# Kernel tuning notes

Measured on AMD Instinct MI355X. Metric: run time of the kernel, lower is better.

Reference implementation:

```python
import jax, jax.numpy as jnp
import numpy as np

ATT = 256
NUM_GENES = 2128
HIDDEN = 512
B, T = 128, 1024


def setup_inputs() -> dict:
    key = jax.random.key(0)
    ks = jax.random.split(key, 8)
    return {
        "genes": jax.random.normal(ks[0], (B, NUM_GENES), dtype=jnp.float32),
        "smiles": jax.random.normal(ks[1], (B, T, HIDDEN), dtype=jnp.float32),
        "w_num_gene_features": jax.random.normal(ks[2], (1,), dtype=jnp.float32) * 0.1,
        "w_genes": jax.random.normal(ks[3], (NUM_GENES, ATT), dtype=jnp.float32) * 0.1,
        "b_genes": jax.random.normal(ks[4], (ATT,), dtype=jnp.float32) * 0.1,
        "dense_kernel": jax.random.normal(ks[5], (HIDDEN, ATT), dtype=jnp.float32) * 0.05,
        "dense_bias": jnp.zeros((ATT,), dtype=jnp.float32),
        "v": jax.random.normal(ks[6], (ATT,), dtype=jnp.float32) * 0.1,
    }


def reference(genes, smiles, w_num_gene_features, w_genes, b_genes,
              dense_kernel, dense_bias, v):
    # genes: [B, G]; collapse trivial feature axis via scalar weight -> [B, G]
    genes_collapsed = genes * w_num_gene_features[0]
    # gene context: [B, A]
    gene_proj = genes_collapsed @ w_genes + b_genes
    # smiles projection: [B, T, A]
    smiles_proj = jnp.einsum('bth,ha->bta', smiles, dense_kernel) + dense_bias
    # additive attention energies
    x = jnp.tanh(gene_proj[:, None, :] + smiles_proj)          # [B, T, A]
    xv = jnp.einsum('bta,a->bt', x, v)                          # [B, T]
    alphas = jax.nn.softmax(xv, axis=-1)                        # [B, T]
    output = jnp.einsum('bth,bt->bh', smiles, alphas)           # [B, H]
    return output, alphas
```

## Files before the change

kernel.cpp:

```cpp
#include <hip/hip_runtime.h>
#include <stdint.h>

#define B_ 128
#define T_ 1024
#define H_ 512
#define A_ 256
#define G_ 2128

typedef short s16x8 __attribute__((ext_vector_type(8)));
typedef float f32x4 __attribute__((ext_vector_type(4)));
typedef unsigned int u32;

__device__ inline unsigned short f2bf(float f) {
  unsigned u = __float_as_uint(f);
  u += 0x7fff + ((u >> 16) & 1);
  return (unsigned short)(u >> 16);
}
__device__ inline unsigned pack2bf(float a, float b) {
  return ((unsigned)f2bf(b) << 16) | f2bf(a);
}
__device__ inline float bf_lo(unsigned u) { return __uint_as_float(u << 16); }
__device__ inline float bf_hi(unsigned u) { return __uint_as_float(u & 0xffff0000u); }
__device__ inline float fast_tanh(float x) {
  x = fminf(15.f, fmaxf(-15.f, x));
  float e = __expf(2.f * x);
  return (e - 1.f) * __builtin_amdgcn_rcpf(e + 1.f);
}
__device__ inline void gl_lds16(const void* g, void* l) {
  __builtin_amdgcn_global_load_lds(
      (const __attribute__((address_space(1))) u32*)g,
      (__attribute__((address_space(3))) u32*)l, 16, 0, 0);
}

__global__ void prep_kt(const float* __restrict__ K,
                        unsigned short* __restrict__ khi) {
  int idx = blockIdx.x * 256 + threadIdx.x;
  int h = idx >> 8;
  int a = idx & 255;
  int kb = h >> 5, k = h & 31;
  int grp = k >> 3, sub = k & 7;
  khi[kb * 8192 + a * 32 + ((grp ^ (a & 3)) * 8) + sub] = f2bf(K[idx]);
}

__global__ __launch_bounds__(256) void gene_proj_k(
    const float* __restrict__ genes, const float* __restrict__ w0p,
    const float* __restrict__ Wg, const float* __restrict__ bg,
    const float* __restrict__ db, float* __restrict__ gp) {
  __shared__ float sg[532];
  int b = blockIdx.x;
  int gc = blockIdx.y;
  int a = threadIdx.x;
  int g0 = gc * 532;
  for (int i = threadIdx.x; i < 532; i += 256) sg[i] = genes[(size_t)b * G_ + g0 + i];
  __syncthreads();
  float s = 0.f;
  #pragma unroll 8
  for (int g = 0; g < 532; ++g)
    s = fmaf(sg[g], Wg[(size_t)(g0 + g) * A_ + a], s);
  float val = w0p[0] * s;
  if (gc == 0) val += bg[a] + db[a];
  atomicAdd(&gp[b * A_ + a], val);
}

__global__ __launch_bounds__(256, 4) void pass1(
    const float* __restrict__ smiles, const unsigned short* __restrict__ khi,
    unsigned short* __restrict__ smb, const float* __restrict__ gp,
    const float* __restrict__ v, float* __restrict__ xv) {
  __shared__ unsigned short sA[64 * 32];
  __shared__ unsigned short sB[256 * 32];
  __shared__ float sXV[64 * 4];

  const int tid = threadIdx.x;
  const int b = blockIdx.y;
  const int tb = blockIdx.x;
  const int lane = tid & 63;
  const int w = tid >> 6;
  const int n = lane & 15;
  const int q = lane >> 4;

  const int ar = tid >> 2;
  const int ac = tid & 3;
  const int swg = (ac ^ (ar & 3)) * 8;
  const float* asrc = smiles + ((size_t)(b * 1024 + tb * 64 + ar)) * 512 + ac * 8;
  unsigned short* adst =
      smb + ((((size_t)(b * 16 + tb)) * 16 * 64 + ar) * 32) + swg;

  f32x4 acc[4][4];
  #pragma unroll
  for (int i = 0; i < 4; ++i)
    #pragma unroll
    for (int j = 0; j < 4; ++j)
      acc[i][j] = (f32x4){0.f, 0.f, 0.f, 0.f};

  float4 f0 = *reinterpret_cast<const float4*>(asrc);
  float4 f1 = *reinterpret_cast<const float4*>(asrc + 4);

  for (int kb = 0; kb < 16; ++kb) {
    __syncthreads();
    uint4 p;
    p.x = pack2bf(f0.x, f0.y); p.y = pack2bf(f0.z, f0.w);
    p.z = pack2bf(f1.x, f1.y); p.w = pack2bf(f1.z, f1.w);
    *reinterpret_cast<uint4*>(&sA[ar * 32 + swg]) = p;
    *reinterpret_cast<uint4*>(adst + kb * 2048) = p;
    #pragma unroll
    for (int r = 0; r < 4; ++r)
      gl_lds16(khi + kb * 8192 + w * 2048 + r * 512 + lane * 8,
               &sB[w * 2048 + r * 512]);
    __syncthreads();
    if (kb < 15) {
      f0 = *reinterpret_cast<const float4*>(asrc + (kb + 1) * 32);
      f1 = *reinterpret_cast<const float4*>(asrc + (kb + 1) * 32 + 4);
    }

    s16x8 af[4], bh[4];
    const int sw = (q ^ (n & 3)) * 8;
    #pragma unroll
    for (int i = 0; i < 4; ++i)
      af[i] = *reinterpret_cast<const s16x8*>(&sA[(i * 16 + n) * 32 + sw]);
    #pragma unroll
    for (int j = 0; j < 4; ++j)
      bh[j] = *reinterpret_cast<const s16x8*>(&sB[(w * 64 + j * 16 + n) * 32 + sw]);
    #pragma unroll
    for (int i = 0; i < 4; ++i)
      #pragma unroll
      for (int j = 0; j < 4; ++j)
        acc[i][j] = __builtin_amdgcn_mfma_f32_16x16x32_bf16(af[i], bh[j], acc[i][j], 0, 0, 0);
  }

  float vv[4], gg[4];
  #pragma unroll
  for (int j = 0; j < 4; ++j) {
    int a = w * 64 + j * 16 + n;
    vv[j] = v[a];
    gg[j] = gp[b * A_ + a];
  }
  #pragma unroll
  for (int i = 0; i < 4; ++i) {
    #pragma unroll
    for (int r = 0; r < 4; ++r) {
      float s = 0.f;
      #pragma unroll
      for (int j = 0; j < 4; ++j)
        s += vv[j] * fast_tanh(acc[i][j][r] + gg[j]);
      s += __shfl_xor(s, 1); s += __shfl_xor(s, 2);
      s += __shfl_xor(s, 4); s += __shfl_xor(s, 8);
      if (n == 0) sXV[(i * 16 + q * 4 + r) * 4 + w] = s;
    }
  }
  __syncthreads();
  if (tid < 64) {
    float* p = &sXV[tid * 4];
    xv[(size_t)b * T_ + tb * 64 + tid] = p[0] + p[1] + p[2] + p[3];
  }
}

__global__ __launch_bounds__(256) void softmax_k(const float* __restrict__ xv,
                                                 float* __restrict__ alphas) {
  __shared__ float red[8];
  int b = blockIdx.x, tid = threadIdx.x;
  float4 x = *reinterpret_cast<const float4*>(xv + b * T_ + tid * 4);
  float m = fmaxf(fmaxf(x.x, x.y), fmaxf(x.z, x.w));
  #pragma unroll
  for (int o = 1; o < 64; o <<= 1) m = fmaxf(m, __shfl_xor(m, o));
  if ((tid & 63) == 0) red[tid >> 6] = m;
  __syncthreads();
  m = fmaxf(fmaxf(red[0], red[1]), fmaxf(red[2], red[3]));
  float e0 = __expf(x.x - m), e1 = __expf(x.y - m);
  float e2 = __expf(x.z - m), e3 = __expf(x.w - m);
  float s = e0 + e1 + e2 + e3;
  #pragma unroll
  for (int o = 1; o < 64; o <<= 1) s += __shfl_xor(s, o);
  if ((tid & 63) == 0) red[4 + (tid >> 6)] = s;
  __syncthreads();
  s = red[4] + red[5] + red[6] + red[7];
  float inv = 1.f / s;
  float4 o4;
  o4.x = e0 * inv; o4.y = e1 * inv; o4.z = e2 * inv; o4.w = e3 * inv;
  *reinterpret_cast<float4*>(alphas + b * T_ + tid * 4) = o4;
}

__global__ __launch_bounds__(256) void pass3(const unsigned short* __restrict__ smb,
                                             const float* __restrict__ alphas,
                                             float* __restrict__ out) {
  __shared__ float red[3][64][8];
  int b = blockIdx.y, ts = blockIdx.x;
  int tid = threadIdx.x;
  int hg = tid & 63, tq = tid >> 6;
  int kb = hg >> 2, g = hg & 3;
  float acc[8] = {0.f, 0.f, 0.f, 0.f, 0.f, 0.f, 0.f, 0.f};
  for (int tb = ts * 4; tb < ts * 4 + 4; ++tb) {
    const unsigned short* tile = smb + (((size_t)b * 16 + tb) * 16 + kb) * 2048;
    const float* al = alphas + b * T_ + tb * 64;
    #pragma unroll 4
    for (int tt = 0; tt < 16; ++tt) {
      int tp = tq * 16 + tt;
      float a = al[tp];
      uint4 d = *reinterpret_cast<const uint4*>(tile + tp * 32 + ((g ^ (tp & 3)) * 8));
      acc[0] = fmaf(a, bf_lo(d.x), acc[0]); acc[1] = fmaf(a, bf_hi(d.x), acc[1]);
      acc[2] = fmaf(a, bf_lo(d.y), acc[2]); acc[3] = fmaf(a, bf_hi(d.y), acc[3]);
      acc[4] = fmaf(a, bf_lo(d.z), acc[4]); acc[5] = fmaf(a, bf_hi(d.z), acc[5]);
      acc[6] = fmaf(a, bf_lo(d.w), acc[6]); acc[7] = fmaf(a, bf_hi(d.w), acc[7]);
    }
  }
  if (tq) {
    #pragma unroll
    for (int e = 0; e < 8; ++e) red[tq - 1][hg][e] = acc[e];
  }
  __syncthreads();
  if (tq == 0) {
    float* op = out + (size_t)b * H_ + kb * 32 + g * 8;
    #pragma unroll
    for (int e = 0; e < 8; ++e)
      atomicAdd(op + e, acc[e] + red[0][hg][e] + red[1][hg][e] + red[2][hg][e]);
  }
}

extern "C" void kernel_launch(void* const* d_in, const int* in_sizes, int n_in,
                              void* d_out, int out_size, void* d_ws, size_t ws_size,
                              hipStream_t stream) {
  const float* genes  = (const float*)d_in[0];
  const float* smiles = (const float*)d_in[1];
  const float* w0     = (const float*)d_in[2];
  const float* wg     = (const float*)d_in[3];
  const float* bg     = (const float*)d_in[4];
  const float* dk     = (const float*)d_in[5];
  const float* db     = (const float*)d_in[6];
  const float* v      = (const float*)d_in[7];
  float* out = (float*)d_out;
  char* ws = (char*)d_ws;
  float* gp = (float*)ws;
  unsigned short* khi = (unsigned short*)(ws + 131072);
  float* xv = (float*)(ws + 131072 + 262144);
  unsigned short* smb = (unsigned short*)(ws + (1 << 20));
  float* alphas = out + B_ * H_;

  hipMemsetAsync(gp, 0, B_ * A_ * sizeof(float), stream);
  hipMemsetAsync(out, 0, B_ * H_ * sizeof(float), stream);
  prep_kt<<<512, 256, 0, stream>>>(dk, khi);
  gene_proj_k<<<dim3(B_, 4), 256, 0, stream>>>(genes, w0, wg, bg, db, gp);
  pass1<<<dim3(16, B_), 256, 0, stream>>>(smiles, khi, smb, gp, v, xv);
  softmax_k<<<B_, 256, 0, stream>>>(xv, alphas);
  pass3<<<dim3(4, B_), 256, 0, stream>>>(smb, alphas, out);
}
```

Before: 507.3 us.

## Double pass1 row tile to 128 and replace gene_proj atomics with partial buffers

```diff
diff --git a/kernel.cpp b/kernel.cpp
--- a/kernel.cpp
+++ b/kernel.cpp
@@ -45,7 +45,7 @@
 __global__ __launch_bounds__(256) void gene_proj_k(
     const float* __restrict__ genes, const float* __restrict__ w0p,
     const float* __restrict__ Wg, const float* __restrict__ bg,
-    const float* __restrict__ db, float* __restrict__ gp) {
+    const float* __restrict__ db, float* __restrict__ gp4) {
   __shared__ float sg[532];
   int b = blockIdx.x;
   int gc = blockIdx.y;
@@ -59,16 +59,16 @@
     s = fmaf(sg[g], Wg[(size_t)(g0 + g) * A_ + a], s);
   float val = w0p[0] * s;
   if (gc == 0) val += bg[a] + db[a];
-  atomicAdd(&gp[b * A_ + a], val);
-}
-
-__global__ __launch_bounds__(256, 4) void pass1(
+  gp4[(gc * B_ + b) * A_ + a] = val;
+}
+
+__global__ __launch_bounds__(256, 2) void pass1(
     const float* __restrict__ smiles, const unsigned short* __restrict__ khi,
-    unsigned short* __restrict__ smb, const float* __restrict__ gp,
+    unsigned short* __restrict__ smb, const float* __restrict__ gp4,
     const float* __restrict__ v, float* __restrict__ xv) {
-  __shared__ unsigned short sA[64 * 32];
+  __shared__ unsigned short sA[128 * 32];
   __shared__ unsigned short sB[256 * 32];
-  __shared__ float sXV[64 * 4];
+  __shared__ float sXV[128 * 4];
 
   const int tid = threadIdx.x;
   const int b = blockIdx.y;
@@ -78,30 +78,37 @@
   const int n = lane & 15;
   const int q = lane >> 4;
 
-  const int ar = tid >> 2;
-  const int ac = tid & 3;
-  const int swg = (ac ^ (ar & 3)) * 8;
-  const float* asrc = smiles + ((size_t)(b * 1024 + tb * 64 + ar)) * 512 + ac * 8;
-  unsigned short* adst =
-      smb + ((((size_t)(b * 16 + tb)) * 16 * 64 + ar) * 32) + swg;
-
-  f32x4 acc[4][4];
-  #pragma unroll
-  for (int i = 0; i < 4; ++i)
+  const int ar = tid >> 1;
+  const int half = tid & 1;
+  const int g0 = half * 2;
+  const int s0 = (g0 ^ (ar & 3)) * 8;
+  const int s1 = ((g0 + 1) ^ (ar & 3)) * 8;
+  const float* asrc = smiles + ((size_t)(b * 1024 + tb * 128 + ar)) * 512 + half * 16;
+  unsigned short* adst = smb + (((size_t)(b * 8 + tb)) * 16) * 4096 + ar * 32;
+
+  f32x4 acc[8][4];
+  #pragma unroll
+  for (int i = 0; i < 8; ++i)
     #pragma unroll
     for (int j = 0; j < 4; ++j)
       acc[i][j] = (f32x4){0.f, 0.f, 0.f, 0.f};
 
   float4 f0 = *reinterpret_cast<const float4*>(asrc);
   float4 f1 = *reinterpret_cast<const float4*>(asrc + 4);
+  float4 f2 = *reinterpret_cast<const float4*>(asrc + 8);
+  float4 f3 = *reinterpret_cast<const float4*>(asrc + 12);
 
   for (int kb = 0; kb < 16; ++kb) {
     __syncthreads();
-    uint4 p;
-    p.x = pack2bf(f0.x, f0.y); p.y = pack2bf(f0.z, f0.w);
-    p.z = pack2bf(f1.x, f1.y); p.w = pack2bf(f1.z, f1.w);
-    *reinterpret_cast<uint4*>(&sA[ar * 32 + swg]) = p;
-    *reinterpret_cast<uint4*>(adst + kb * 2048) = p;
+    uint4 p0, p1;
+    p0.x = pack2bf(f0.x, f0.y); p0.y = pack2bf(f0.z, f0.w);
+    p0.z = pack2bf(f1.x, f1.y); p0.w = pack2bf(f1.z, f1.w);
+    p1.x = pack2bf(f2.x, f2.y); p1.y = pack2bf(f2.z, f2.w);
+    p1.z = pack2bf(f3.x, f3.y); p1.w = pack2bf(f3.z, f3.w);
+    *reinterpret_cast<uint4*>(&sA[ar * 32 + s0]) = p0;
+    *reinterpret_cast<uint4*>(&sA[ar * 32 + s1]) = p1;
+    *reinterpret_cast<uint4*>(adst + kb * 4096 + s0) = p0;
+    *reinterpret_cast<uint4*>(adst + kb * 4096 + s1) = p1;
     #pragma unroll
     for (int r = 0; r < 4; ++r)
       gl_lds16(khi + kb * 8192 + w * 2048 + r * 512 + lane * 8,
@@ -110,18 +117,20 @@
     if (kb < 15) {
       f0 = *reinterpret_cast<const float4*>(asrc + (kb + 1) * 32);
       f1 = *reinterpret_cast<const float4*>(asrc + (kb + 1) * 32 + 4);
+      f2 = *reinterpret_cast<const float4*>(asrc + (kb + 1) * 32 + 8);
+      f3 = *reinterpret_cast<const float4*>(asrc + (kb + 1) * 32 + 12);
     }
 
-    s16x8 af[4], bh[4];
+    s16x8 af[8], bh[4];
     const int sw = (q ^ (n & 3)) * 8;
-    #pragma unroll
-    for (int i = 0; i < 4; ++i)
-      af[i] = *reinterpret_cast<const s16x8*>(&sA[(i * 16 + n) * 32 + sw]);
     #pragma unroll
     for (int j = 0; j < 4; ++j)
       bh[j] = *reinterpret_cast<const s16x8*>(&sB[(w * 64 + j * 16 + n) * 32 + sw]);
     #pragma unroll
-    for (int i = 0; i < 4; ++i)
+    for (int i = 0; i < 8; ++i)
+      af[i] = *reinterpret_cast<const s16x8*>(&sA[(i * 16 + n) * 32 + sw]);
+    #pragma unroll
+    for (int i = 0; i < 8; ++i)
       #pragma unroll
       for (int j = 0; j < 4; ++j)
         acc[i][j] = __builtin_amdgcn_mfma_f32_16x16x32_bf16(af[i], bh[j], acc[i][j], 0, 0, 0);
@@ -131,11 +140,13 @@
   #pragma unroll
   for (int j = 0; j < 4; ++j) {
     int a = w * 64 + j * 16 + n;
+    int idx = b * A_ + a;
     vv[j] = v[a];
-    gg[j] = gp[b * A_ + a];
-  }
-  #pragma unroll
-  for (int i = 0; i < 4; ++i) {
+    gg[j] = gp4[idx] + gp4[B_ * A_ + idx] + gp4[2 * B_ * A_ + idx] +
+            gp4[3 * B_ * A_ + idx];
+  }
+  #pragma unroll
+  for (int i = 0; i < 8; ++i) {
     #pragma unroll
     for (int r = 0; r < 4; ++r) {
       float s = 0.f;
@@ -148,9 +159,9 @@
     }
   }
   __syncthreads();
-  if (tid < 64) {
+  if (tid < 128) {
     float* p = &sXV[tid * 4];
-    xv[(size_t)b * T_ + tb * 64 + tid] = p[0] + p[1] + p[2] + p[3];
+    xv[(size_t)b * T_ + tb * 128 + tid] = p[0] + p[1] + p[2] + p[3];
   }
 }
 
@@ -188,12 +199,12 @@
   int hg = tid & 63, tq = tid >> 6;
   int kb = hg >> 2, g = hg & 3;
   float acc[8] = {0.f, 0.f, 0.f, 0.f, 0.f, 0.f, 0.f, 0.f};
-  for (int tb = ts * 4; tb < ts * 4 + 4; ++tb) {
-    const unsigned short* tile = smb + (((size_t)b * 16 + tb) * 16 + kb) * 2048;
-    const float* al = alphas + b * T_ + tb * 64;
+  for (int tb = ts * 2; tb < ts * 2 + 2; ++tb) {
+    const unsigned short* tile = smb + (((size_t)b * 8 + tb) * 16 + kb) * 4096;
+    const float* al = alphas + b * T_ + tb * 128;
     #pragma unroll 4
-    for (int tt = 0; tt < 16; ++tt) {
-      int tp = tq * 16 + tt;
+    for (int tt = 0; tt < 32; ++tt) {
+      int tp = tq * 32 + tt;
       float a = al[tp];
       uint4 d = *reinterpret_cast<const uint4*>(tile + tp * 32 + ((g ^ (tp & 3)) * 8));
       acc[0] = fmaf(a, bf_lo(d.x), acc[0]); acc[1] = fmaf(a, bf_hi(d.x), acc[1]);
@@ -228,17 +239,16 @@
   const float* v      = (const float*)d_in[7];
   float* out = (float*)d_out;
   char* ws = (char*)d_ws;
-  float* gp = (float*)ws;
-  unsigned short* khi = (unsigned short*)(ws + 131072);
-  float* xv = (float*)(ws + 131072 + 262144);
-  unsigned short* smb = (unsigned short*)(ws + (1 << 20));
+  float* gp4 = (float*)ws;
+  unsigned short* khi = (unsigned short*)(ws + 524288);
+  float* xv = (float*)(ws + 524288 + 262144);
+  unsigned short* smb = (unsigned short*)(ws + (2 << 20));
   float* alphas = out + B_ * H_;
 
-  hipMemsetAsync(gp, 0, B_ * A_ * sizeof(float), stream);
   hipMemsetAsync(out, 0, B_ * H_ * sizeof(float), stream);
   prep_kt<<<512, 256, 0, stream>>>(dk, khi);
-  gene_proj_k<<<dim3(B_, 4), 256, 0, stream>>>(genes, w0, wg, bg, db, gp);
-  pass1<<<dim3(16, B_), 256, 0, stream>>>(smiles, khi, smb, gp, v, xv);
+  gene_proj_k<<<dim3(B_, 4), 256, 0, stream>>>(genes, w0, wg, bg, db, gp4);
+  pass1<<<dim3(8, B_), 256, 0, stream>>>(smiles, khi, smb, gp4, v, xv);
   softmax_k<<<B_, 256, 0, stream>>>(xv, alphas);
   pass3<<<dim3(4, B_), 256, 0, stream>>>(smb, alphas, out);
 }
```

Result: no change. 499.5 us (-1.5%).
